# Optimization experiments

Hardware: AMD Instinct MI355X
Metric: run time of the kernel (lower is better)

Reference implementation:

```python
import jax, jax.numpy as jnp
import numpy as np

ROPE_BASE = 10000.0

def apply_rope(x, offset=0):
    # x: [B, H, L, Dh], traditional (interleaved-pair) RoPE
    B, H, L, Dh = x.shape
    pos = jnp.arange(L, dtype=jnp.float32) + offset            # [L]
    freqs = ROPE_BASE ** (-jnp.arange(0, Dh, 2, dtype=jnp.float32) / Dh)  # [Dh/2]
    theta = pos[:, None] * freqs[None, :]                      # [L, Dh/2]
    cos, sin = jnp.cos(theta), jnp.sin(theta)
    x1 = x[..., 0::2]                                          # [B,H,L,Dh/2]
    x2 = x[..., 1::2]
    r1 = x1 * cos - x2 * sin
    r2 = x1 * sin + x2 * cos
    return jnp.stack([r1, r2], axis=-1).reshape(B, H, L, Dh)


def setup_inputs() -> dict:
    key = jax.random.key(0)
    ks = jax.random.split(key, 5)
    B, L, D = 2, 2048, 2048
    s = 1.0 / np.sqrt(D)
    x = jax.random.normal(ks[0], (B, L, D), dtype=jnp.float32)
    # additive causal mask (0 on/below diagonal, -1e9 above)
    mask = jnp.where(jnp.tril(jnp.ones((L, L), dtype=bool)), 0.0, -1e9).astype(jnp.float32)
    Wq = jax.random.normal(ks[1], (D, D), dtype=jnp.float32) * s
    Wk = jax.random.normal(ks[2], (D, D), dtype=jnp.float32) * s
    Wv = jax.random.normal(ks[3], (D, D), dtype=jnp.float32) * s
    Wo = jax.random.normal(ks[4], (D, D), dtype=jnp.float32) * s
    return {"x": x, "mask": mask, "Wq": Wq, "Wk": Wk, "Wv": Wv, "Wo": Wo}


def reference(x, mask, Wq, Wk, Wv, Wo):
    num_heads = 16
    B, L, D = x.shape
    Dh = D // num_heads
    q = (x @ Wq.T).reshape(B, L, num_heads, Dh).transpose(0, 2, 1, 3)  # [B,H,L,Dh]
    k = (x @ Wk.T).reshape(B, L, num_heads, Dh).transpose(0, 2, 1, 3)
    v = (x @ Wv.T).reshape(B, L, num_heads, Dh).transpose(0, 2, 1, 3)
    q = apply_rope(q)
    k = apply_rope(k)
    scale = 1.0 / jnp.sqrt(jnp.float32(Dh))
    scores = jnp.einsum('bhqd,bhkd->bhqk', q * scale, k) + mask  # [B,H,L,L]
    probs = jax.nn.softmax(scores, axis=-1)
    vh = jnp.einsum('bhqk,bhkd->bhqd', probs, v)                 # [B,H,L,Dh]
    vh = vh.transpose(0, 2, 1, 3).reshape(B, L, D)
    out = vh @ Wo.T
    return out, k, v
```

## Files before the change

### kernel.cpp

```cpp
#include <hip/hip_runtime.h>

typedef __attribute__((ext_vector_type(4))) float f32x4;
typedef __attribute__((ext_vector_type(8))) __bf16 bf16x8;

__device__ __forceinline__ unsigned short f2b(float f) {
  unsigned int u = __builtin_bit_cast(unsigned int, f);
  u = (u + 0x7fffu + ((u >> 16) & 1u)) >> 16;
  return (unsigned short)u;
}
__device__ __forceinline__ float b2f(unsigned short h) {
  unsigned int u = ((unsigned int)h) << 16;
  return __builtin_bit_cast(float, u);
}
__device__ __forceinline__ void gl_lds16(const void* g, void* l) {
  __builtin_amdgcn_global_load_lds(
      (const __attribute__((address_space(1))) void*)g,
      (__attribute__((address_space(3))) void*)l, 16, 0, 0);
}

__global__ void cast_kernel(const float* __restrict__ src,
                            unsigned short* __restrict__ dst, int n4) {
  int i = blockIdx.x * blockDim.x + threadIdx.x;
  if (i >= n4) return;
  float4 v = ((const float4*)src)[i];
  ushort4 o;
  o.x = f2b(v.x); o.y = f2b(v.y); o.z = f2b(v.z); o.w = f2b(v.w);
  ((ushort4*)dst)[i] = o;
}

__global__ void cast4_kernel(const float* __restrict__ s0, const float* __restrict__ s1,
                             const float* __restrict__ s2, const float* __restrict__ s3,
                             unsigned short* __restrict__ d0, unsigned short* __restrict__ d1,
                             unsigned short* __restrict__ d2, unsigned short* __restrict__ d3,
                             int n4) {
  int i = blockIdx.x * blockDim.x + threadIdx.x;
  if (i >= n4) return;
  const float* src = blockIdx.y == 0 ? s0 : blockIdx.y == 1 ? s1 : blockIdx.y == 2 ? s2 : s3;
  unsigned short* dst = blockIdx.y == 0 ? d0 : blockIdx.y == 1 ? d1 : blockIdx.y == 2 ? d2 : d3;
  float4 v = ((const float4*)src)[i];
  ushort4 o;
  o.x = f2b(v.x); o.y = f2b(v.y); o.z = f2b(v.z); o.w = f2b(v.w);
  ((ushort4*)dst)[i] = o;
}

__global__ void rope_table_kernel(float2* __restrict__ tab) {
  int idx = blockIdx.x * blockDim.x + threadIdx.x;
  int l = idx >> 6, i = idx & 63;
  float freq = powf(10000.0f, -(float)(2 * i) / 128.0f);
  float th = (float)l * freq;
  tab[idx] = make_float2(cosf(th), sinf(th));
}

__global__ void rope_apply_kernel(unsigned short* __restrict__ qb,
                                  unsigned short* __restrict__ kb,
                                  unsigned short* __restrict__ vb,
                                  float* __restrict__ kout,
                                  float* __restrict__ vout,
                                  const float2* __restrict__ tab) {
  const float QS = 0.12751743f;
  int z = blockIdx.y;
  int p = blockIdx.x * blockDim.x + threadIdx.x;
  int i = p & 63;
  int t = p >> 6;
  int h = t & 15; t >>= 4;
  int l = t & 2047;
  int b = t >> 11;
  int base = ((b * 2048 + l) * 2048) + h * 128 + 2 * i;
  int obase = ((b * 16 + h) * 2048 + l) * 128 + 2 * i;
  if (z == 2) {
    vout[obase] = b2f(vb[base]);
    vout[obase + 1] = b2f(vb[base + 1]);
  } else {
    unsigned short* buf = z ? kb : qb;
    float x1 = b2f(buf[base]), x2 = b2f(buf[base + 1]);
    float2 cs = tab[l * 64 + i];
    float r1 = x1 * cs.x - x2 * cs.y;
    float r2 = x1 * cs.y + x2 * cs.x;
    if (z == 1) {
      buf[base] = f2b(r1);
      buf[base + 1] = f2b(r2);
      kout[obase] = r1; kout[obase + 1] = r2;
    } else {
      buf[base] = f2b(r1 * QS);
      buf[base + 1] = f2b(r2 * QS);
    }
  }
}

__global__ __launch_bounds__(256) void transpose_v_kernel(const unsigned short* __restrict__ vb,
                                                          unsigned short* __restrict__ vt) {
  __shared__ unsigned short t[32][33];
  int bz = blockIdx.z;
  int b = bz >> 4, h = bz & 15;
  int l0 = blockIdx.x * 32, d0 = blockIdx.y * 32;
  const unsigned short* src = vb + (size_t)b * 2048 * 2048 + h * 128;
  unsigned short* dst = vt + (size_t)bz * 128 * 2048;
  int tx = threadIdx.x & 31, ty = threadIdx.x >> 5;
#pragma unroll
  for (int i = 0; i < 4; ++i)
    t[ty + 8 * i][tx] = src[(size_t)(l0 + ty + 8 * i) * 2048 + d0 + tx];
  __syncthreads();
#pragma unroll
  for (int i = 0; i < 4; ++i)
    dst[(size_t)(d0 + ty + 8 * i) * 2048 + l0 + tx] = t[tx][ty + 8 * i];
}

template <int BM, int NBN, int OUT_F32>
__global__ __launch_bounds__(512, 2) void gemm3(const unsigned short* __restrict__ A,
                                                const unsigned short* __restrict__ W,
                                                void* __restrict__ C) {
  constexpr int K = 2048, NT = 32;
  constexpr int AH = BM / 2;
  constexpr int MF = BM / 64;
  constexpr int AQ = AH / 64;
  __shared__ unsigned short Asm[2][2][AH * 64];
  __shared__ unsigned short Bsm[2][2][128 * 64];

  const int tid = threadIdx.x, lane = tid & 63, wv = tid >> 6;
  const int wr = wv >> 2, wc = wv & 3;
  const int ln = lane & 15, kg = lane >> 4;

  const int cpx = (int)gridDim.x >> 3;
  const int swzb = ((int)blockIdx.x & 7) * cpx + ((int)blockIdx.x >> 3);
  const int bm = swzb / NBN, bn = swzb % NBN;
  const int m0 = bm * BM, n0 = bn * 256;

  const int rr = lane >> 3;
  const int sws = ((lane & 7) ^ (rr & 7)) * 8;
  const unsigned short* pA = A + (size_t)(m0 + wv * 8 * AQ + rr) * K + sws;
  const unsigned short* pB = W + (size_t)(n0 + wv * 16 + rr) * K + sws;

#define STA_(dd, hh, tt)                                                         \
  _Pragma("unroll") for (int q = 0; q < AQ; ++q)                                 \
      gl_lds16(pA + ((size_t)(hh)*AH + q * 8) * K + (size_t)(tt)*64,             \
               &Asm[dd][hh][(wv * 8 * AQ + q * 8) * 64 + lane * 8]);
#define STB_(dd, hh, tt)                                                         \
  _Pragma("unroll") for (int q = 0; q < 2; ++q)                                  \
      gl_lds16(pB + ((size_t)(hh)*128 + q * 8) * K + (size_t)(tt)*64,            \
               &Bsm[dd][hh][(wv * 16 + q * 8) * 64 + lane * 8]);

  const int sw0 = (kg ^ (ln & 7)) * 8;
  const int sw1 = ((4 + kg) ^ (ln & 7)) * 8;
  const int rae = (wr * (AH / 2) + ln) * 64;
  const int rbe = (wc * 32 + ln) * 64;

  f32x4 acc[2 * MF][4] = {};
  bf16x8 aA[MF][2], bB[2][2];

#define QUAD(dd, mh, bh, LA, LB)                                                  \
  {                                                                               \
    if (LA) {                                                                     \
      _Pragma("unroll") for (int mf = 0; mf < MF; ++mf) {                         \
        aA[mf][0] = *(const bf16x8*)&Asm[dd][mh][rae + mf * 1024 + sw0];          \
        aA[mf][1] = *(const bf16x8*)&Asm[dd][mh][rae + mf * 1024 + sw1];          \
      }                                                                           \
    }                                                                             \
    if (LB) {                                                                     \
      _Pragma("unroll") for (int nf = 0; nf < 2; ++nf) {                          \
        bB[nf][0] = *(const bf16x8*)&Bsm[dd][bh][rbe + nf * 1024 + sw0];          \
        bB[nf][1] = *(const bf16x8*)&Bsm[dd][bh][rbe + nf * 1024 + sw1];          \
      }                                                                           \
    }                                                                             \
    __builtin_amdgcn_s_setprio(1);                                                \
    _Pragma("unroll") for (int mf = 0; mf < MF; ++mf)                             \
        _Pragma("unroll") for (int nf = 0; nf < 2; ++nf) {                        \
      acc[(mh)*MF + mf][(bh)*2 + nf] = __builtin_amdgcn_mfma_f32_16x16x32_bf16(   \
          aA[mf][0], bB[nf][0], acc[(mh)*MF + mf][(bh)*2 + nf], 0, 0, 0);         \
      acc[(mh)*MF + mf][(bh)*2 + nf] = __builtin_amdgcn_mfma_f32_16x16x32_bf16(   \
          aA[mf][1], bB[nf][1], acc[(mh)*MF + mf][(bh)*2 + nf], 0, 0, 0);         \
    }                                                                             \
    __builtin_amdgcn_s_setprio(0);                                                \
  }

#define BAR                                                                       \
  __builtin_amdgcn_s_barrier();                                                   \
  __builtin_amdgcn_sched_barrier(0);
#define VWAIT                                                                     \
  if (BM == 256) { asm volatile("s_waitcnt vmcnt(4)" ::: "memory"); }             \
  else { asm volatile("s_waitcnt vmcnt(3)" ::: "memory"); }

  STA_(0, 0, 0); STB_(0, 0, 0); STB_(0, 1, 0); STA_(0, 1, 0);
  STA_(1, 0, 1); STB_(1, 1, 1);
  VWAIT; BAR;

  for (int T = 0; T < NT; T += 2) {
    const bool more = (T + 2) < NT;
    STB_(1, 0, T + 1);            QUAD(0, 0, 0, 1, 1); BAR;
    STA_(1, 1, T + 1);            QUAD(0, 0, 1, 0, 1); BAR;
    if (more) STA_(0, 0, T + 2);  QUAD(0, 1, 1, 1, 0); BAR;
    if (more) STB_(0, 1, T + 2);  QUAD(0, 1, 0, 0, 1);
    if (more) { VWAIT; } else { asm volatile("s_waitcnt vmcnt(0)" ::: "memory"); }
    BAR;
    if (more) STB_(0, 0, T + 2);  QUAD(1, 0, 0, 1, 1); BAR;
    if (more) STA_(0, 1, T + 2);  QUAD(1, 0, 1, 0, 1); BAR;
    if (more) STA_(1, 0, T + 3);  QUAD(1, 1, 1, 1, 0); BAR;
    if (more) {
      STB_(1, 1, T + 3);          QUAD(1, 1, 0, 0, 1); VWAIT; BAR;
    } else {
      QUAD(1, 1, 0, 0, 1);
    }
  }

  const int mat = bn >> 3;
  unsigned short* Cb = (unsigned short*)C;
  float* Cf = (float*)C;
#pragma unroll
  for (int mh = 0; mh < 2; ++mh)
#pragma unroll
    for (int mf = 0; mf < MF; ++mf)
#pragma unroll
      for (int j = 0; j < 4; ++j) {
        int row = m0 + mh * AH + wr * (AH / 2) + mf * 16 + kg * 4 + j;
        size_t rb = (size_t)mat * 8388608 + (size_t)row * 2048 + (size_t)((bn & 7) * 256);
#pragma unroll
        for (int bh = 0; bh < 2; ++bh)
#pragma unroll
          for (int nf = 0; nf < 2; ++nf) {
            int col = bh * 128 + wc * 32 + nf * 16 + ln;
            float v = acc[mh * MF + mf][bh * 2 + nf][j];
            if (OUT_F32) Cf[rb + col] = v;
            else Cb[rb + col] = f2b(v);
          }
      }
#undef STA_
#undef STB_
#undef QUAD
#undef BAR
#undef VWAIT
}

__global__ __launch_bounds__(256, 2) void attn3_kernel(const unsigned short* __restrict__ Qb,
                                                       const unsigned short* __restrict__ Kb,
                                                       const unsigned short* __restrict__ Vt,
                                                       unsigned short* __restrict__ Ob) {
  __shared__ unsigned short KS[2][8192];
  __shared__ unsigned short VS[2][8192];
  __shared__ unsigned short PS[4][2048];
  const int D = 2048, L = 2048;
  int tid = threadIdx.x, lane = tid & 63, w = tid >> 6;
  int ln = lane & 15, kg = lane >> 4;
  int bid = blockIdx.x;
  int g = bid >> 5, bh = bid & 31;
  int qt = (g < 8) ? (15 - g) : (g - 8);
  int b = bh >> 4, h = bh & 15;
  const size_t base = (size_t)b * L * D + h * 128;
  const unsigned short* Kp = Kb + base;
  const unsigned short* Qp = Qb + base;
  unsigned short* Op = Ob + base;
  const unsigned short* Vp = Vt + (size_t)bh * 128 * L;

  int q0 = qt * 128;
  int qw0 = q0 + w * 32;

  bf16x8 aq[2][4];
#pragma unroll
  for (int m = 0; m < 2; ++m)
#pragma unroll
    for (int kc = 0; kc < 4; ++kc)
      aq[m][kc] = *(const bf16x8*)&Qp[(size_t)(qw0 + m * 16 + ln) * D + kc * 32 + kg * 8];

  f32x4 o[2][8] = {};
  float m2[2][4], ls[2][4];
#pragma unroll
  for (int m = 0; m < 2; ++m)
#pragma unroll
    for (int j = 0; j < 4; ++j) { m2[m][j] = -1e30f; ls[m][j] = 0.f; }

  int l16 = lane >> 4, l8 = lane >> 3, l7 = lane & 7;

#define STAGE(T, NB)                                                                   \
  {                                                                                    \
    int kv0_ = (T) << 6;                                                               \
    _Pragma("unroll") for (int i = 0; i < 4; ++i) {                                    \
      int cK = w * 4 + i;                                                              \
      int r = cK * 4 + l16;                                                            \
      int sw = ln ^ (r & 7);                                                           \
      gl_lds16(Kp + (size_t)(kv0_ + r) * D + sw * 8, &KS[NB][cK * 512 + lane * 8]);    \
      int dh = cK * 8 + l8;                                                            \
      int sv = l7 ^ (dh & 7);                                                          \
      gl_lds16(Vp + (size_t)dh * L + kv0_ + sv * 8, &VS[NB][cK * 512 + lane * 8]);     \
    }                                                                                  \
  }

  int nt = 2 * qt + 2;
  int mask_t = 2 * qt + (w >> 1);

  STAGE(0, 0);
  __syncthreads();

  for (int t = 0; t < nt; ++t) {
    int cur = t & 1;
    if (t + 1 < nt) STAGE(t + 1, cur ^ 1);

    if (t <= mask_t) {
      int kv0 = t << 6;
      f32x4 s[2][4] = {};
#pragma unroll
      for (int n = 0; n < 4; ++n)
#pragma unroll
        for (int kc = 0; kc < 4; ++kc) {
          bf16x8 bk = *(const bf16x8*)&KS[cur][(n * 16 + ln) * 128 + (((kc << 2) + kg) ^ (ln & 7)) * 8];
          s[0][n] = __builtin_amdgcn_mfma_f32_16x16x32_bf16(aq[0][kc], bk, s[0][n], 0, 0, 0);
          s[1][n] = __builtin_amdgcn_mfma_f32_16x16x32_bf16(aq[1][kc], bk, s[1][n], 0, 0, 0);
        }
      if (t == mask_t) {
#pragma unroll
        for (int m = 0; m < 2; ++m)
#pragma unroll
          for (int n = 0; n < 4; ++n)
#pragma unroll
            for (int j = 0; j < 4; ++j)
              if (kv0 + n * 16 + ln > qw0 + m * 16 + kg * 4 + j) s[m][n][j] = -1e30f;
      }
      float pmax[2][4];
      bool near = true;
#pragma unroll
      for (int m = 0; m < 2; ++m)
#pragma unroll
        for (int j = 0; j < 4; ++j) {
          pmax[m][j] = fmaxf(fmaxf(s[m][0][j], s[m][1][j]), fmaxf(s[m][2][j], s[m][3][j]));
          near = near && (pmax[m][j] <= m2[m][j] + 8.0f);
        }
      if (!__all(near)) {
#pragma unroll
        for (int m = 0; m < 2; ++m)
#pragma unroll
          for (int j = 0; j < 4; ++j) {
            float mx = pmax[m][j];
#pragma unroll
            for (int d = 1; d < 16; d <<= 1) mx = fmaxf(mx, __shfl_xor(mx, d));
            mx = fmaxf(mx, m2[m][j]);
            float al = __builtin_amdgcn_exp2f(m2[m][j] - mx);
            m2[m][j] = mx;
            ls[m][j] *= al;
#pragma unroll
            for (int dt = 0; dt < 8; ++dt) o[m][dt][j] *= al;
          }
      }
#pragma unroll
      for (int m = 0; m < 2; ++m)
#pragma unroll
        for (int j = 0; j < 4; ++j) {
          int row = m * 16 + kg * 4 + j;
          float acc = 0.f;
#pragma unroll
          for (int n = 0; n < 4; ++n) {
            float p = __builtin_amdgcn_exp2f(s[m][n][j] - m2[m][j]);
            acc += p;
            unsigned int u = __builtin_bit_cast(unsigned int, p);
            PS[w][row * 64 + (((n * 2 + (ln >> 3)) ^ (row & 7)) * 8) + (ln & 7)] =
                (unsigned short)(u >> 16);
          }
          ls[m][j] += acc;
        }
#pragma unroll
      for (int kst = 0; kst < 2; ++kst) {
        bf16x8 ap0 = *(const bf16x8*)&PS[w][(ln) * 64 + (((kst << 2) + kg) ^ (ln & 7)) * 8];
        bf16x8 ap1 = *(const bf16x8*)&PS[w][(16 + ln) * 64 + (((kst << 2) + kg) ^ (ln & 7)) * 8];
#pragma unroll
        for (int dt = 0; dt < 8; ++dt) {
          bf16x8 bv = *(const bf16x8*)&VS[cur][(dt * 16 + ln) * 64 + (((kst << 2) + kg) ^ (ln & 7)) * 8];
          o[0][dt] = __builtin_amdgcn_mfma_f32_16x16x32_bf16(ap0, bv, o[0][dt], 0, 0, 0);
          o[1][dt] = __builtin_amdgcn_mfma_f32_16x16x32_bf16(ap1, bv, o[1][dt], 0, 0, 0);
        }
      }
    }
    __syncthreads();
  }
#undef STAGE

#pragma unroll
  for (int m = 0; m < 2; ++m)
#pragma unroll
    for (int j = 0; j < 4; ++j) {
      float tsum = ls[m][j];
#pragma unroll
      for (int d = 1; d < 16; d <<= 1) tsum += __shfl_xor(tsum, d);
      float inv = 1.0f / tsum;
      int row = qw0 + m * 16 + kg * 4 + j;
#pragma unroll
      for (int dt = 0; dt < 8; ++dt)
        Op[(size_t)row * D + dt * 16 + ln] = f2b(o[m][dt][j] * inv);
    }
}

extern "C" void kernel_launch(void* const* d_in, const int* in_sizes, int n_in,
                              void* d_out, int out_size, void* d_ws, size_t ws_size,
                              hipStream_t stream) {
  const float* x  = (const float*)d_in[0];
  const float* Wq = (const float*)d_in[2];
  const float* Wk = (const float*)d_in[3];
  const float* Wv = (const float*)d_in[4];
  const float* Wo = (const float*)d_in[5];

  char* ws = (char*)d_ws;
  unsigned short* xb  = (unsigned short*)(ws + 0);
  unsigned short* wqb = (unsigned short*)(ws + 16777216);
  unsigned short* wkb = (unsigned short*)(ws + 25165824);
  unsigned short* wvb = (unsigned short*)(ws + 33554432);
  unsigned short* wob = (unsigned short*)(ws + 41943040);
  unsigned short* qb  = (unsigned short*)(ws + 50331648);
  unsigned short* kb  = (unsigned short*)(ws + 67108864);
  unsigned short* vb  = (unsigned short*)(ws + 83886080);
  float2* tab         = (float2*)(ws + 100663296);
  unsigned short* vt  = wqb;
  unsigned short* ob  = xb;

  float* out  = (float*)d_out;
  float* kout = out + 8388608;
  float* vout = out + 16777216;

  cast_kernel<<<8192, 256, 0, stream>>>(x, xb, 2097152);
  cast4_kernel<<<dim3(4096, 4), 256, 0, stream>>>(Wq, Wk, Wv, Wo, wqb, wkb, wvb, wob, 1048576);
  rope_table_kernel<<<512, 256, 0, stream>>>(tab);

  gemm3<256, 24, 0><<<384, 512, 0, stream>>>(xb, wqb, qb);

  transpose_v_kernel<<<dim3(64, 4, 32), 256, 0, stream>>>(vb, vt);

  rope_apply_kernel<<<dim3(16384, 3), 256, 0, stream>>>(qb, kb, vb, kout, vout, tab);

  attn3_kernel<<<512, 256, 0, stream>>>(qb, kb, vt, ob);

  gemm3<128, 8, 1><<<256, 512, 0, stream>>>(ob, wob, out);
}
```

Before: 327.9 us.

## Restructure GEMM main loop into 8-wave ping-pong with split LDS loads and MFMA phases

Splits the per-quadrant LDS fragment loads out of the compute block and brackets each MFMA cluster with barriers, giving an HipKittens-style 8-wave ping-pong. The B fragments are double-buffered per half so loads for the next quadrant can be issued ahead of the barrier and the MFMA phase. The goal is to overlap LDS reads and global-to-LDS copies with matrix math across the two waves sharing a SIMD. The trade-off is twice as many barriers per iteration and more registers for the B fragments. The ordering of async global-to-LDS stores against the shared-buffer reads also has to stay correct.

```diff
diff --git a/kernel.cpp b/kernel.cpp
--- a/kernel.cpp
+++ b/kernel.cpp
@@ -106,7 +106,7 @@
 }
 
 template <int BM, int NBN, int OUT_F32>
-__global__ __launch_bounds__(512, 2) void gemm3(const unsigned short* __restrict__ A,
+__global__ __launch_bounds__(512, 2) void gemm4(const unsigned short* __restrict__ A,
                                                 const unsigned short* __restrict__ W,
                                                 void* __restrict__ C) {
   constexpr int K = 2048, NT = 32;
@@ -131,13 +131,13 @@
   const unsigned short* pB = W + (size_t)(n0 + wv * 16 + rr) * K + sws;
 
 #define STA_(dd, hh, tt)                                                         \
-  _Pragma("unroll") for (int q = 0; q < AQ; ++q)                                 \
+  { _Pragma("unroll") for (int q = 0; q < AQ; ++q)                               \
       gl_lds16(pA + ((size_t)(hh)*AH + q * 8) * K + (size_t)(tt)*64,             \
-               &Asm[dd][hh][(wv * 8 * AQ + q * 8) * 64 + lane * 8]);
+               &Asm[dd][hh][(wv * 8 * AQ + q * 8) * 64 + lane * 8]); }
 #define STB_(dd, hh, tt)                                                         \
-  _Pragma("unroll") for (int q = 0; q < 2; ++q)                                  \
+  { _Pragma("unroll") for (int q = 0; q < 2; ++q)                                \
       gl_lds16(pB + ((size_t)(hh)*128 + q * 8) * K + (size_t)(tt)*64,            \
-               &Bsm[dd][hh][(wv * 16 + q * 8) * 64 + lane * 8]);
+               &Bsm[dd][hh][(wv * 16 + q * 8) * 64 + lane * 8]); }
 
   const int sw0 = (kg ^ (ln & 7)) * 8;
   const int sw1 = ((4 + kg) ^ (ln & 7)) * 8;
@@ -145,60 +145,66 @@
   const int rbe = (wc * 32 + ln) * 64;
 
   f32x4 acc[2 * MF][4] = {};
-  bf16x8 aA[MF][2], bB[2][2];
-
-#define QUAD(dd, mh, bh, LA, LB)                                                  \
+  bf16x8 aA[MF][2], bB[2][2][2];
+
+#define LDA_(dd, mh)                                                              \
+  { _Pragma("unroll") for (int mf = 0; mf < MF; ++mf) {                           \
+      aA[mf][0] = *(const bf16x8*)&Asm[dd][mh][rae + mf * 1024 + sw0];            \
+      aA[mf][1] = *(const bf16x8*)&Asm[dd][mh][rae + mf * 1024 + sw1];            \
+    } }
+#define LDB_(dd, bh)                                                              \
+  { _Pragma("unroll") for (int nf = 0; nf < 2; ++nf) {                            \
+      bB[bh][nf][0] = *(const bf16x8*)&Bsm[dd][bh][rbe + nf * 1024 + sw0];        \
+      bB[bh][nf][1] = *(const bf16x8*)&Bsm[dd][bh][rbe + nf * 1024 + sw1];        \
+    } }
+
+#define QMM(mh, bh)                                                               \
   {                                                                               \
-    if (LA) {                                                                     \
-      _Pragma("unroll") for (int mf = 0; mf < MF; ++mf) {                         \
-        aA[mf][0] = *(const bf16x8*)&Asm[dd][mh][rae + mf * 1024 + sw0];          \
-        aA[mf][1] = *(const bf16x8*)&Asm[dd][mh][rae + mf * 1024 + sw1];          \
-      }                                                                           \
-    }                                                                             \
-    if (LB) {                                                                     \
-      _Pragma("unroll") for (int nf = 0; nf < 2; ++nf) {                          \
-        bB[nf][0] = *(const bf16x8*)&Bsm[dd][bh][rbe + nf * 1024 + sw0];          \
-        bB[nf][1] = *(const bf16x8*)&Bsm[dd][bh][rbe + nf * 1024 + sw1];          \
-      }                                                                           \
-    }                                                                             \
     __builtin_amdgcn_s_setprio(1);                                                \
     _Pragma("unroll") for (int mf = 0; mf < MF; ++mf)                             \
         _Pragma("unroll") for (int nf = 0; nf < 2; ++nf) {                        \
       acc[(mh)*MF + mf][(bh)*2 + nf] = __builtin_amdgcn_mfma_f32_16x16x32_bf16(   \
-          aA[mf][0], bB[nf][0], acc[(mh)*MF + mf][(bh)*2 + nf], 0, 0, 0);         \
+          aA[mf][0], bB[bh][nf][0], acc[(mh)*MF + mf][(bh)*2 + nf], 0, 0, 0);     \
       acc[(mh)*MF + mf][(bh)*2 + nf] = __builtin_amdgcn_mfma_f32_16x16x32_bf16(   \
-          aA[mf][1], bB[nf][1], acc[(mh)*MF + mf][(bh)*2 + nf], 0, 0, 0);         \
+          aA[mf][1], bB[bh][nf][1], acc[(mh)*MF + mf][(bh)*2 + nf], 0, 0, 0);     \
     }                                                                             \
     __builtin_amdgcn_s_setprio(0);                                                \
   }
 
-#define BAR                                                                       \
-  __builtin_amdgcn_s_barrier();                                                   \
-  __builtin_amdgcn_sched_barrier(0);
+#define BAR   { __builtin_amdgcn_s_barrier(); __builtin_amdgcn_sched_barrier(0); }
 #define VWAIT                                                                     \
-  if (BM == 256) { asm volatile("s_waitcnt vmcnt(4)" ::: "memory"); }             \
-  else { asm volatile("s_waitcnt vmcnt(3)" ::: "memory"); }
+  { if (BM == 256) { asm volatile("s_waitcnt vmcnt(4)" ::: "memory"); }           \
+    else { asm volatile("s_waitcnt vmcnt(3)" ::: "memory"); } }
+#define VW0   { asm volatile("s_waitcnt vmcnt(0)" ::: "memory"); }
 
   STA_(0, 0, 0); STB_(0, 0, 0); STB_(0, 1, 0); STA_(0, 1, 0);
   STA_(1, 0, 1); STB_(1, 1, 1);
-  VWAIT; BAR;
+  VWAIT;
 
   for (int T = 0; T < NT; T += 2) {
     const bool more = (T + 2) < NT;
-    STB_(1, 0, T + 1);            QUAD(0, 0, 0, 1, 1); BAR;
-    STA_(1, 1, T + 1);            QUAD(0, 0, 1, 0, 1); BAR;
-    if (more) STA_(0, 0, T + 2);  QUAD(0, 1, 1, 1, 0); BAR;
-    if (more) STB_(0, 1, T + 2);  QUAD(0, 1, 0, 0, 1);
-    if (more) { VWAIT; } else { asm volatile("s_waitcnt vmcnt(0)" ::: "memory"); }
-    BAR;
-    if (more) STB_(0, 0, T + 2);  QUAD(1, 0, 0, 1, 1); BAR;
-    if (more) STA_(0, 1, T + 2);  QUAD(1, 0, 1, 0, 1); BAR;
-    if (more) STA_(1, 0, T + 3);  QUAD(1, 1, 1, 1, 0); BAR;
-    if (more) {
-      STB_(1, 1, T + 3);          QUAD(1, 1, 0, 0, 1); VWAIT; BAR;
-    } else {
-      QUAD(1, 1, 0, 0, 1);
-    }
+    LDA_(0, 0); LDB_(0, 0);
+    STB_(1, 0, T + 1);
+    BAR; QMM(0, 0); BAR;
+    LDB_(0, 1);
+    STA_(1, 1, T + 1);
+    BAR; QMM(0, 1); BAR;
+    LDA_(0, 1);
+    if (more) STA_(0, 0, T + 2);
+    BAR; QMM(1, 1); BAR;
+    if (more) { STB_(0, 1, T + 2); VWAIT; } else { VW0; }
+    BAR; QMM(1, 0); BAR;
+    LDA_(1, 0); LDB_(1, 0);
+    if (more) STB_(0, 0, T + 2);
+    BAR; QMM(0, 0); BAR;
+    LDB_(1, 1);
+    if (more) STA_(0, 1, T + 2);
+    BAR; QMM(0, 1); BAR;
+    LDA_(1, 1);
+    if (more) STA_(1, 0, T + 3);
+    BAR; QMM(1, 1); BAR;
+    if (more) { STB_(1, 1, T + 3); VWAIT; }
+    BAR; QMM(1, 0); BAR;
   }
 
   const int mat = bn >> 3;
@@ -224,9 +230,12 @@
       }
 #undef STA_
 #undef STB_
-#undef QUAD
+#undef LDA_
+#undef LDB_
+#undef QMM
 #undef BAR
 #undef VWAIT
+#undef VW0
 }
 
 __global__ __launch_bounds__(256, 2) void attn3_kernel(const unsigned short* __restrict__ Qb,
@@ -414,7 +423,7 @@
   cast4_kernel<<<dim3(4096, 4), 256, 0, stream>>>(Wq, Wk, Wv, Wo, wqb, wkb, wvb, wob, 1048576);
   rope_table_kernel<<<512, 256, 0, stream>>>(tab);
 
-  gemm3<256, 24, 0><<<384, 512, 0, stream>>>(xb, wqb, qb);
+  gemm4<256, 24, 0><<<384, 512, 0, stream>>>(xb, wqb, qb);
 
   transpose_v_kernel<<<dim3(64, 4, 32), 256, 0, stream>>>(vb, vt);
 
@@ -422,5 +431,5 @@
 
   attn3_kernel<<<512, 256, 0, stream>>>(qb, kb, vt, ob);
 
-  gemm3<128, 8, 1><<<256, 512, 0, stream>>>(ob, wob, out);
-}
+  gemm4<128, 8, 1><<<256, 512, 0, stream>>>(ob, wob, out);
+}
```

New measurement: 306.6 us. 1.07x faster.
